# Optimization experiments

Hardware: AMD Instinct MI355X
Metric: run time of the kernel (lower is better)

The kernel has to match this reference:

```python
import jax, jax.numpy as jnp
import numpy as np

N_NODES = 50000
N_EDGES = 800000
HIDDEN = 128
BN_EPS = 1e-5
LEAKY_SLOPE = 0.01


def setup_inputs() -> dict:
    key = jax.random.key(0)
    ks = jax.random.split(key, 8)
    x = jax.random.normal(ks[0], (N_NODES, HIDDEN), dtype=jnp.float32)
    edge_index = jax.random.randint(ks[1], (2, N_EDGES), 0, N_NODES, dtype=jnp.int64)
    # stacked per-layer params (4 SAGEConv layers, all 128->128)
    sc = 1.0 / np.sqrt(HIDDEN)
    Wl = jax.random.normal(ks[2], (4, HIDDEN, HIDDEN), dtype=jnp.float32) * sc
    bl = jax.random.normal(ks[3], (4, HIDDEN), dtype=jnp.float32) * sc
    Wr = jax.random.normal(ks[4], (4, HIDDEN, HIDDEN), dtype=jnp.float32) * sc
    gamma = jnp.ones((4, HIDDEN), dtype=jnp.float32)
    beta = jnp.zeros((4, HIDDEN), dtype=jnp.float32)
    return {"x": x, "edge_index": edge_index, "Wl": Wl, "bl": bl,
            "Wr": Wr, "gamma": gamma, "beta": beta}


def _sage_mean_agg(x, src, dst, n):
    # gather source features per edge, scatter-mean onto destination nodes
    msg = x[src]                                                  # [E, F]
    agg = jax.ops.segment_sum(msg, dst, num_segments=n)           # [N, F]
    cnt = jax.ops.segment_sum(jnp.ones_like(dst, dtype=x.dtype), dst, num_segments=n)
    return agg / jnp.maximum(cnt, 1.0)[:, None]


def _bn_train(x, g, b):
    mu = jnp.mean(x, axis=0)
    var = jnp.mean((x - mu) ** 2, axis=0)  # biased variance (PyTorch BN normalization)
    return (x - mu) * jax.lax.rsqrt(var + BN_EPS) * g + b


def reference(x, edge_index, Wl, bl, Wr, gamma, beta):
    src, dst = edge_index[0], edge_index[1]
    n = x.shape[0]
    h = x
    for i in range(4):
        agg = _sage_mean_agg(h, src, dst, n)
        h = agg @ Wl[i] + bl[i] + h @ Wr[i]          # SAGEConv: lin_l(mean_nbr) + lin_r(root)
        h = jnp.where(h >= 0, h, LEAKY_SLOPE * h)    # leaky_relu
        h = _bn_train(h, gamma[i], beta[i])
    # dropout: eval-mode identity (deterministic reference)
    return h
```

## Files before the change

### kernel.cpp

```cpp
#include <hip/hip_runtime.h>
#include <hip/hip_bf16.h>

#define N_NODES 50000
#define N_EDGES 800000
#define F 128
#define BN_EPS 1e-5f
#define SLOPE 0.01f
#define NB 782
#define CAP 64
#define NBIN 128
#define BINSZ 391
#define QCAP2 8192
#define ABLK 512
#define AITER 7
#define PB1 6250
#define PB2 512

typedef __attribute__((ext_vector_type(8))) __bf16 bf16x8_t;
typedef __attribute__((ext_vector_type(8))) unsigned short u16x8_t;
typedef __attribute__((ext_vector_type(4))) float f32x4_t;

__device__ __forceinline__ unsigned short f2b(float f) {
    unsigned int u = __float_as_uint(f);
    unsigned int r = (u + 0x7fffu + ((u >> 16) & 1u)) >> 16;
    return (unsigned short)r;
}
__device__ __forceinline__ float b2f_lo(unsigned int v) { return __uint_as_float(v << 16); }
__device__ __forceinline__ float b2f_hi(unsigned int v) { return __uint_as_float(v & 0xffff0000u); }


__global__ __launch_bounds__(256) void bucket2_kernel(const int* __restrict__ src,
                                                      const int* __restrict__ dst,
                                                      int* __restrict__ qtail,
                                                      unsigned int* __restrict__ qdata) {
    __shared__ int counts[NBIN];
    __shared__ int cur[NBIN];
    __shared__ int base[NBIN];
    const int tid = threadIdx.x;

    for (int k = tid; k < NBIN; k += 256) { counts[k] = 0; cur[k] = 0; }
    __syncthreads();

    unsigned int pack[AITER];
    int bin[AITER];
    const int stride = ABLK * 256;
#pragma unroll
    for (int it = 0; it < AITER; ++it) {
        const int e = blockIdx.x * 256 + tid + it * stride;
        bin[it] = -1;
        if (e < N_EDGES) {
            int d = __builtin_nontemporal_load(dst + e);
            int s = __builtin_nontemporal_load(src + e);
            bin[it] = d / BINSZ;
            pack[it] = ((unsigned int)d << 16) | (unsigned int)s;
            atomicAdd(&counts[bin[it]], 1);
        }
    }
    __syncthreads();
    if (tid < NBIN) {
        int c = counts[tid];
        base[tid] = (c > 0) ? atomicAdd(&qtail[tid * 16], c) : 0;
    }
    __syncthreads();
#pragma unroll
    for (int it = 0; it < AITER; ++it) {
        if (bin[it] >= 0) {
            int slot = base[bin[it]] + atomicAdd(&cur[bin[it]], 1);
            qdata[(long)bin[it] * QCAP2 + slot] = pack[it];
        }
    }
}

__global__ __launch_bounds__(256) void scatter2_kernel(const unsigned int* __restrict__ qdata,
                                                       const int* __restrict__ qtail,
                                                       int* __restrict__ deg,
                                                       unsigned short* __restrict__ csr) {
    __shared__ int cnt[BINSZ];
    __shared__ unsigned short stage[BINSZ][CAP];
    const int b = blockIdx.x;
    const int nbase = b * BINSZ;
    const int nn = min(BINSZ, N_NODES - nbase);
    const int tid = threadIdx.x;

    for (int r = tid; r < BINSZ; r += 256) cnt[r] = 0;
    __syncthreads();

    const int n = qtail[b * 16];
    const unsigned int* q = qdata + (long)b * QCAP2;
    for (int i = tid; i < n; i += 256) {
        unsigned int p = q[i];
        int local = (int)(p >> 16) - nbase;
        int pos = atomicAdd(&cnt[local], 1);
        if (pos < CAP) stage[local][pos] = (unsigned short)(p & 0xffff);
    }
    __syncthreads();

    for (int c = tid; c < nn * (CAP / 8); c += 256) {
        const int r = c >> 3;
        const int col = (c & 7) * 8;
        *(u16x8_t*)(csr + (long)(nbase + r) * CAP + col) = *(const u16x8_t*)&stage[r][col];
    }
    for (int r = tid; r < nn; r += 256) deg[nbase + r] = min(cnt[r], CAP);
}


__global__ __launch_bounds__(256) void prep_kernel(const float* __restrict__ x,
                                                   unsigned short* __restrict__ hb,
                                                   const float* __restrict__ Wl,
                                                   const float* __restrict__ Wr,
                                                   unsigned short* __restrict__ Wt,
                                                   float* __restrict__ scale,
                                                   float* __restrict__ shift) {
    const int b = blockIdx.x;
    const int tid = threadIdx.x;
    if (b < PB1) {
        long i = (long)b * 256 + tid;
        float4 v = ((const float4*)x)[i];
        ushort4 o;
        o.x = f2b(v.x); o.y = f2b(v.y); o.z = f2b(v.z); o.w = f2b(v.w);
        ((ushort4*)hb)[i] = o;
    } else if (b < PB1 + PB2) {
        int idx = (b - PB1) * 256 + tid;
        int k = idx & 255;
        int n = (idx >> 8) & 127;
        int i = idx >> 15;
        float v = (k < F) ? Wl[((long)i * F + k) * F + n]
                          : Wr[((long)i * F + (k - F)) * F + n];
        Wt[idx] = f2b(v);
    } else {
        if (tid < F) { scale[tid] = 1.f; shift[tid] = 0.f; }
    }
}


__device__ __forceinline__ u16x8_t affine8(u16x8_t av, const float* __restrict__ sc,
                                           const float* __restrict__ sh) {
    u16x8_t r;
#pragma unroll
    for (int j = 0; j < 8; ++j) {
        float v = __uint_as_float(((unsigned int)av[j]) << 16);
        v = v * sc[j] + sh[j];
        r[j] = f2b(v);
    }
    return r;
}

#define ACC8(A, V)                               \
    A[0] += b2f_lo(V.x); A[1] += b2f_hi(V.x);    \
    A[2] += b2f_lo(V.y); A[3] += b2f_hi(V.y);    \
    A[4] += b2f_lo(V.z); A[5] += b2f_hi(V.z);    \
    A[6] += b2f_lo(V.w); A[7] += b2f_hi(V.w);

#define PACKJ(j, A) {                                                   \
    const float4 s0 = *(const float4*)(scale + q * 8 + 32 * (j));       \
    const float4 s1 = *(const float4*)(scale + q * 8 + 32 * (j) + 4);   \
    const float4 t0 = *(const float4*)(shift + q * 8 + 32 * (j));       \
    const float4 t1 = *(const float4*)(shift + q * 8 + 32 * (j) + 4);   \
    u16x8_t r;                                                          \
    r[0] = f2b(A[0] * inv * s0.x + t0.x);                               \
    r[1] = f2b(A[1] * inv * s0.y + t0.y);                               \
    r[2] = f2b(A[2] * inv * s0.z + t0.z);                               \
    r[3] = f2b(A[3] * inv * s0.w + t0.w);                               \
    r[4] = f2b(A[4] * inv * s1.x + t1.x);                               \
    r[5] = f2b(A[5] * inv * s1.y + t1.y);                               \
    r[6] = f2b(A[6] * inv * s1.z + t1.z);                               \
    r[7] = f2b(A[7] * inv * s1.w + t1.w);                               \
    areg[j] = r; }

#if __has_builtin(__builtin_amdgcn_global_load_lds)
#define STAGE_HALF(half) {                                                        \
    _Pragma("unroll")                                                             \
    for (int f = 0; f < 8; ++f) {                                                 \
        const int fid = f * 256 + tid;                                            \
        const int lf = fid & 63;                                                  \
        const int ksf = (fid >> 6) & 3;                                           \
        const int ntf = fid >> 8;                                                 \
        const int n = ntf * 16 + (lf & 15);                                       \
        const int k = (half) * 128 + ksf * 32 + (lf >> 4) * 8;                    \
        const unsigned short* gsrc = Wt + (long)n * 256 + k;                      \
        unsigned short* lbase = stage + (f * 256 + wave * 64) * 8;                \
        __builtin_amdgcn_global_load_lds(                                         \
            (const __attribute__((address_space(1))) void*)gsrc,                  \
            (__attribute__((address_space(3))) void*)lbase, 16, 0, 0);            \
    } }
#else
#define STAGE_HALF(half) {                                                        \
    _Pragma("unroll")                                                             \
    for (int f = 0; f < 8; ++f) {                                                 \
        const int fid = f * 256 + tid;                                            \
        const int lf = fid & 63;                                                  \
        const int ksf = (fid >> 6) & 3;                                           \
        const int ntf = fid >> 8;                                                 \
        const int n = ntf * 16 + (lf & 15);                                       \
        const int k = (half) * 128 + ksf * 32 + (lf >> 4) * 8;                    \
        const unsigned short* gsrc = Wt + (long)n * 256 + k;                      \
        *(u16x8_t*)(stage + fid * 8) = *(const u16x8_t*)gsrc;                     \
    } }
#endif

__global__ __launch_bounds__(256) void gemm_fused(const unsigned short* __restrict__ hin,
                                                  const int* __restrict__ deg,
                                                  const unsigned short* __restrict__ csr,
                                                  const float* __restrict__ scale,
                                                  const float* __restrict__ shift,
                                                  const unsigned short* __restrict__ Wt,
                                                  const float* __restrict__ bl,
                                                  unsigned short* __restrict__ Pb,
                                                  float* __restrict__ partial) {
    __shared__ __align__(16) char shraw[32768];
    unsigned short* stage = (unsigned short*)shraw;
    unsigned short* ep16 = (unsigned short*)shraw;
    __shared__ float lsum[4][F];
    __shared__ float lsq[4][F];

    const int tid = threadIdx.x;
    const int wave = tid >> 6, lane = tid & 63;
    const int m = lane & 15, q = lane >> 4;
    const int rbase = blockIdx.x * 64 + wave * 16;
    const int arow = rbase + m;
    const bool aval = arow < N_NODES;

    STAGE_HALF(0);

    const unsigned short* hp = hin + (long)arow * F + q * 8;
    u16x8_t hraw[4];
#pragma unroll
    for (int j = 0; j < 4; ++j) hraw[j] = (u16x8_t)0;
    if (aval) {
#pragma unroll
        for (int j = 0; j < 4; ++j) hraw[j] = *(const u16x8_t*)(hp + j * 32);
    }

    const int d = aval ? deg[arow] : 0;
    const unsigned short* crow = csr + (long)arow * CAP;
    const unsigned short* hq = hin + q * 8;
    float a0[8], a1[8], a2[8], a3[8];
#pragma unroll
    for (int j = 0; j < 8; ++j) { a0[j] = 0.f; a1[j] = 0.f; a2[j] = 0.f; a3[j] = 0.f; }

    const int d4 = d & ~3;
    for (int e = 0; e < d4; e += 4) {
        const ushort4 iv = *(const ushort4*)(crow + e);
        const unsigned short* r0 = hq + (long)iv.x * F;
        const unsigned short* r1 = hq + (long)iv.y * F;
        const unsigned short* r2 = hq + (long)iv.z * F;
        const unsigned short* r3 = hq + (long)iv.w * F;
        uint4 v00 = *(const uint4*)(r0);
        uint4 v01 = *(const uint4*)(r0 + 32);
        uint4 v02 = *(const uint4*)(r0 + 64);
        uint4 v03 = *(const uint4*)(r0 + 96);
        uint4 v10 = *(const uint4*)(r1);
        uint4 v11 = *(const uint4*)(r1 + 32);
        uint4 v12 = *(const uint4*)(r1 + 64);
        uint4 v13 = *(const uint4*)(r1 + 96);
        uint4 v20 = *(const uint4*)(r2);
        uint4 v21 = *(const uint4*)(r2 + 32);
        uint4 v22 = *(const uint4*)(r2 + 64);
        uint4 v23 = *(const uint4*)(r2 + 96);
        uint4 v30 = *(const uint4*)(r3);
        uint4 v31 = *(const uint4*)(r3 + 32);
        uint4 v32 = *(const uint4*)(r3 + 64);
        uint4 v33 = *(const uint4*)(r3 + 96);
        ACC8(a0, v00); ACC8(a1, v01); ACC8(a2, v02); ACC8(a3, v03);
        ACC8(a0, v10); ACC8(a1, v11); ACC8(a2, v12); ACC8(a3, v13);
        ACC8(a0, v20); ACC8(a1, v21); ACC8(a2, v22); ACC8(a3, v23);
        ACC8(a0, v30); ACC8(a1, v31); ACC8(a2, v32); ACC8(a3, v33);
    }
    for (int e = d4; e < d; ++e) {
        const int s = (int)crow[e];
        const unsigned short* hr = hq + (long)s * F;
        uint4 v0 = *(const uint4*)(hr);
        uint4 v1 = *(const uint4*)(hr + 32);
        uint4 v2 = *(const uint4*)(hr + 64);
        uint4 v3 = *(const uint4*)(hr + 96);
        ACC8(a0, v0);
        ACC8(a1, v1);
        ACC8(a2, v2);
        ACC8(a3, v3);
    }

    u16x8_t areg[8];
#pragma unroll
    for (int j = 0; j < 8; ++j) areg[j] = (u16x8_t)0;
    if (d > 0) {
        const float inv = 1.0f / (float)d;
        PACKJ(0, a0);
        PACKJ(1, a1);
        PACKJ(2, a2);
        PACKJ(3, a3);
    }
    if (aval) {
#pragma unroll
        for (int j = 0; j < 4; ++j) {
            const int base = j * 32 + q * 8;
            areg[4 + j] = affine8(hraw[j], scale + base, shift + base);
        }
    }

    f32x4_t acc[8];
#pragma unroll
    for (int nt = 0; nt < 8; ++nt) acc[nt] = (f32x4_t){0.f, 0.f, 0.f, 0.f};

    __syncthreads();
#pragma unroll
    for (int ks = 0; ks < 4; ++ks) {
        bf16x8_t af = __builtin_bit_cast(bf16x8_t, areg[ks]);
#pragma unroll
        for (int nt = 0; nt < 8; ++nt) {
            u16x8_t bv = *(const u16x8_t*)(stage + ((nt * 4 + ks) * 64 + lane) * 8);
            bf16x8_t bf = __builtin_bit_cast(bf16x8_t, bv);
            acc[nt] = __builtin_amdgcn_mfma_f32_16x16x32_bf16(af, bf, acc[nt], 0, 0, 0);
        }
    }
    __syncthreads();
    STAGE_HALF(1);
    __syncthreads();
#pragma unroll
    for (int ks = 0; ks < 4; ++ks) {
        bf16x8_t af = __builtin_bit_cast(bf16x8_t, areg[4 + ks]);
#pragma unroll
        for (int nt = 0; nt < 8; ++nt) {
            u16x8_t bv = *(const u16x8_t*)(stage + ((nt * 4 + ks) * 64 + lane) * 8);
            bf16x8_t bf = __builtin_bit_cast(bf16x8_t, bv);
            acc[nt] = __builtin_amdgcn_mfma_f32_16x16x32_bf16(af, bf, acc[nt], 0, 0, 0);
        }
    }

    __syncthreads();

    float cs[8], cq[8];
#pragma unroll
    for (int nt = 0; nt < 8; ++nt) {
        cs[nt] = 0.f; cq[nt] = 0.f;
        const int c = nt * 16 + m;
        const float b = bl[c];
#pragma unroll
        for (int r = 0; r < 4; ++r) {
            const int rl = wave * 16 + q * 4 + r;
            float v = acc[nt][r] + b;
            v = (v >= 0.f) ? v : SLOPE * v;
            ep16[rl * 136 + c] = f2b(v);
            if (rbase + q * 4 + r < N_NODES) {
                cs[nt] += v;
                cq[nt] += v * v;
            }
        }
    }

    {
        const int rq = lane >> 4;
        const int cc = (lane & 15) * 8;
#pragma unroll
        for (int r2 = 0; r2 < 4; ++r2) {
            const int rl = wave * 16 + rq * 4 + r2;
            const int grow = blockIdx.x * 64 + rl;
            if (grow < N_NODES)
                *(u16x8_t*)(Pb + (long)grow * F + cc) = *(const u16x8_t*)(ep16 + rl * 136 + cc);
        }
    }

#pragma unroll
    for (int nt = 0; nt < 8; ++nt) {
        cs[nt] += __shfl_xor(cs[nt], 16);
        cs[nt] += __shfl_xor(cs[nt], 32);
        cq[nt] += __shfl_xor(cq[nt], 16);
        cq[nt] += __shfl_xor(cq[nt], 32);
    }
    if (lane < 16) {
#pragma unroll
        for (int nt = 0; nt < 8; ++nt) {
            lsum[wave][nt * 16 + m] = cs[nt];
            lsq[wave][nt * 16 + m] = cq[nt];
        }
    }
    __syncthreads();
    if (tid < F) {
        float s = 0.f, s2 = 0.f;
#pragma unroll
        for (int w = 0; w < 4; ++w) {
            s += lsum[w][tid];
            s2 += lsq[w][tid];
        }
        partial[(long)blockIdx.x * 256 + tid] = s;
        partial[(long)blockIdx.x * 256 + 128 + tid] = s2;
    }
}

__global__ __launch_bounds__(256) void bn_reduce(const float* __restrict__ partial,
                                                 const float* __restrict__ gamma,
                                                 const float* __restrict__ beta,
                                                 float* __restrict__ scale,
                                                 float* __restrict__ shift) {
    const int j = blockIdx.x;
    const int t = threadIdx.x;
    const int lane = t & 63, wave = t >> 6;
    float s = 0.f, s2 = 0.f;
    for (int b = t; b < NB; b += 256) {
        s += partial[(long)b * 256 + j];
        s2 += partial[(long)b * 256 + 128 + j];
    }
#pragma unroll
    for (int off = 1; off < 64; off <<= 1) {
        s += __shfl_xor(s, off);
        s2 += __shfl_xor(s2, off);
    }
    __shared__ float ls[4], lq[4];
    if (lane == 0) { ls[wave] = s; lq[wave] = s2; }
    __syncthreads();
    if (t == 0) {
        float S = ls[0] + ls[1] + ls[2] + ls[3];
        float Q = lq[0] + lq[1] + lq[2] + lq[3];
        const float inv_n = 1.0f / (float)N_NODES;
        float mu = S * inv_n;
        float var = Q * inv_n - mu * mu;
        float scl = gamma[j] * rsqrtf(var + BN_EPS);
        scale[j] = scl;
        shift[j] = beta[j] - mu * scl;
    }
}

__global__ __launch_bounds__(256) void bn_apply_f(const unsigned short* __restrict__ Pb,
                                                  float* __restrict__ out,
                                                  const float* __restrict__ scale,
                                                  const float* __restrict__ shift) {
    long i = (long)blockIdx.x * blockDim.x + threadIdx.x;
    if (i >= (long)N_NODES * (F / 8)) return;
    const int c8 = (int)(i & 15);
    uint4 v = ((const uint4*)Pb)[i];
    const float4 sc0 = ((const float4*)scale)[c8 * 2];
    const float4 sc1 = ((const float4*)scale)[c8 * 2 + 1];
    const float4 sh0 = ((const float4*)shift)[c8 * 2];
    const float4 sh1 = ((const float4*)shift)[c8 * 2 + 1];
    float4 o0, o1;
    o0.x = b2f_lo(v.x) * sc0.x + sh0.x;
    o0.y = b2f_hi(v.x) * sc0.y + sh0.y;
    o0.z = b2f_lo(v.y) * sc0.z + sh0.z;
    o0.w = b2f_hi(v.y) * sc0.w + sh0.w;
    o1.x = b2f_lo(v.z) * sc1.x + sh1.x;
    o1.y = b2f_hi(v.z) * sc1.y + sh1.y;
    o1.z = b2f_lo(v.w) * sc1.z + sh1.z;
    o1.w = b2f_hi(v.w) * sc1.w + sh1.w;
    ((float4*)out)[i * 2] = o0;
    ((float4*)out)[i * 2 + 1] = o1;
}


extern "C" void kernel_launch(void* const* d_in, const int* in_sizes, int n_in,
                              void* d_out, int out_size, void* d_ws, size_t ws_size,
                              hipStream_t stream) {
    const float* x     = (const float*)d_in[0];
    const int*   ei    = (const int*)d_in[1];
    const float* Wl    = (const float*)d_in[2];
    const float* bl    = (const float*)d_in[3];
    const float* Wr    = (const float*)d_in[4];
    const float* gamma = (const float*)d_in[5];
    const float* beta  = (const float*)d_in[6];
    float* out = (float*)d_out;

    const int* src = ei;
    const int* dst = ei + N_EDGES;

    char* w = (char*)d_ws;
    auto alloc = [&](size_t bytes) -> char* {
        char* p = w;
        w += (bytes + 255) & ~(size_t)255;
        return p;
    };
    unsigned short* hbA   = (unsigned short*)alloc((size_t)N_NODES * F * 2);
    unsigned short* hbB   = (unsigned short*)alloc((size_t)N_NODES * F * 2);
    unsigned short* Wt    = (unsigned short*)alloc((size_t)4 * F * 256 * 2);
    int*   deg      = (int*)alloc((size_t)N_NODES * 4);
    int*   qtail    = (int*)alloc((size_t)NBIN * 16 * 4);
    unsigned int* qdata = (unsigned int*)alloc((size_t)NBIN * QCAP2 * 4);
    unsigned short* csr = (unsigned short*)alloc((size_t)N_NODES * CAP * 2);
    float* partial  = (float*)alloc((size_t)NB * 256 * 4);
    float* scale    = (float*)alloc(F * 4);
    float* shift    = (float*)alloc(F * 4);

    hipMemsetAsync(qtail, 0, (size_t)NBIN * 16 * 4, stream);

    bucket2_kernel<<<ABLK, 256, 0, stream>>>(src, dst, qtail, qdata);
    scatter2_kernel<<<NBIN, 256, 0, stream>>>(qdata, qtail, deg, csr);
    prep_kernel<<<PB1 + PB2 + 1, 256, 0, stream>>>(x, hbA, Wl, Wr, Wt, scale, shift);

    const int n8 = N_NODES * (F / 8);

    unsigned short* hin = hbA;
    unsigned short* hnext = hbB;
    for (int i = 0; i < 4; ++i) {
        gemm_fused<<<NB, 256, 0, stream>>>(
            hin, deg, csr, scale, shift, Wt + (size_t)i * F * 256, bl + (size_t)i * F,
            hnext, partial);

        bn_reduce<<<F, 256, 0, stream>>>(partial, gamma + (size_t)i * F, beta + (size_t)i * F,
                                         scale, shift);

        unsigned short* t = hin; hin = hnext; hnext = t;
    }
    bn_apply_f<<<(n8 + 255) / 256, 256, 0, stream>>>(hin, out, scale, shift);
}
```

Measured before the change: 374.5 us.

## Split neighbor aggregation of each 16-row tile across four waves

Each block now handles 16 rows instead of 64, so the grid grows from 782 to 3125 blocks. The four waves split every row's neighbor list into quarters and combine their partial sums with LDS float atomics. Each wave then computes two of the eight output column tiles in the MFMA GEMM. The aim is more parallelism on the latency-bound gather and better load balance across uneven node degrees. In exchange, the 64 KB of weights are staged into LDS four times as often per row, LDS atomics are added, and bn_reduce has more partial rows to sum.

After: 994.9 us. 166% more time.

```diff
diff --git a/kernel.cpp b/kernel.cpp
--- a/kernel.cpp
+++ b/kernel.cpp
@@ -6,7 +6,7 @@
 #define F 128
 #define BN_EPS 1e-5f
 #define SLOPE 0.01f
-#define NB 782
+#define NB2 3125
 #define CAP 64
 #define NBIN 128
 #define BINSZ 391
@@ -76,7 +76,7 @@
                                                        int* __restrict__ deg,
                                                        unsigned short* __restrict__ csr) {
     __shared__ int cnt[BINSZ];
-    __shared__ unsigned short stage[BINSZ][CAP];
+    __shared__ __align__(16) unsigned short stage[BINSZ][CAP];
     const int b = blockIdx.x;
     const int nbase = b * BINSZ;
     const int nn = min(BINSZ, N_NODES - nbase);
@@ -150,22 +150,6 @@
     A[2] += b2f_lo(V.y); A[3] += b2f_hi(V.y);    \
     A[4] += b2f_lo(V.z); A[5] += b2f_hi(V.z);    \
     A[6] += b2f_lo(V.w); A[7] += b2f_hi(V.w);
-
-#define PACKJ(j, A) {                                                   \
-    const float4 s0 = *(const float4*)(scale + q * 8 + 32 * (j));       \
-    const float4 s1 = *(const float4*)(scale + q * 8 + 32 * (j) + 4);   \
-    const float4 t0 = *(const float4*)(shift + q * 8 + 32 * (j));       \
-    const float4 t1 = *(const float4*)(shift + q * 8 + 32 * (j) + 4);   \
-    u16x8_t r;                                                          \
-    r[0] = f2b(A[0] * inv * s0.x + t0.x);                               \
-    r[1] = f2b(A[1] * inv * s0.y + t0.y);                               \
-    r[2] = f2b(A[2] * inv * s0.z + t0.z);                               \
-    r[3] = f2b(A[3] * inv * s0.w + t0.w);                               \
-    r[4] = f2b(A[4] * inv * s1.x + t1.x);                               \
-    r[5] = f2b(A[5] * inv * s1.y + t1.y);                               \
-    r[6] = f2b(A[6] * inv * s1.z + t1.z);                               \
-    r[7] = f2b(A[7] * inv * s1.w + t1.w);                               \
-    areg[j] = r; }
 
 #if __has_builtin(__builtin_amdgcn_global_load_lds)
 #define STAGE_HALF(half) {                                                        \
@@ -198,48 +182,45 @@
     } }
 #endif
 
-__global__ __launch_bounds__(256) void gemm_fused(const unsigned short* __restrict__ hin,
-                                                  const int* __restrict__ deg,
-                                                  const unsigned short* __restrict__ csr,
-                                                  const float* __restrict__ scale,
-                                                  const float* __restrict__ shift,
-                                                  const unsigned short* __restrict__ Wt,
-                                                  const float* __restrict__ bl,
-                                                  unsigned short* __restrict__ Pb,
-                                                  float* __restrict__ partial) {
+__global__ __launch_bounds__(256, 4) void gemm_fused(const unsigned short* __restrict__ hin,
+                                                     const int* __restrict__ deg,
+                                                     const unsigned short* __restrict__ csr,
+                                                     const float* __restrict__ scale,
+                                                     const float* __restrict__ shift,
+                                                     const unsigned short* __restrict__ Wt,
+                                                     const float* __restrict__ bl,
+                                                     unsigned short* __restrict__ Pb,
+                                                     float* __restrict__ partial) {
     __shared__ __align__(16) char shraw[32768];
+    __shared__ __align__(16) float ldsA[2048];
     unsigned short* stage = (unsigned short*)shraw;
-    unsigned short* ep16 = (unsigned short*)shraw;
-    __shared__ float lsum[4][F];
-    __shared__ float lsq[4][F];
+    unsigned short* ep16 = (unsigned short*)ldsA;
 
     const int tid = threadIdx.x;
     const int wave = tid >> 6, lane = tid & 63;
     const int m = lane & 15, q = lane >> 4;
-    const int rbase = blockIdx.x * 64 + wave * 16;
+    const int rbase = blockIdx.x * 16;
     const int arow = rbase + m;
-    const bool aval = arow < N_NODES;
+
+    for (int i = tid; i < 2048; i += 256) ldsA[i] = 0.f;
+    __syncthreads();
 
     STAGE_HALF(0);
 
-    const unsigned short* hp = hin + (long)arow * F + q * 8;
-    u16x8_t hraw[4];
-#pragma unroll
-    for (int j = 0; j < 4; ++j) hraw[j] = (u16x8_t)0;
-    if (aval) {
-#pragma unroll
-        for (int j = 0; j < 4; ++j) hraw[j] = *(const u16x8_t*)(hp + j * 32);
-    }
-
-    const int d = aval ? deg[arow] : 0;
+    const int d = deg[arow];
     const unsigned short* crow = csr + (long)arow * CAP;
     const unsigned short* hq = hin + q * 8;
+
     float a0[8], a1[8], a2[8], a3[8];
 #pragma unroll
     for (int j = 0; j < 8; ++j) { a0[j] = 0.f; a1[j] = 0.f; a2[j] = 0.f; a3[j] = 0.f; }
 
-    const int d4 = d & ~3;
-    for (int e = 0; e < d4; e += 4) {
+    const int qlen = ((d + 15) >> 4) << 2;
+    const int lo = min(wave * qlen, d);
+    const int hi = min(lo + qlen, d);
+    const int nfull = lo + ((hi - lo) & ~3);
+    int e = lo;
+    for (; e < nfull; e += 4) {
         const ushort4 iv = *(const ushort4*)(crow + e);
         const unsigned short* r0 = hq + (long)iv.x * F;
         const unsigned short* r1 = hq + (long)iv.y * F;
@@ -266,123 +247,119 @@
         ACC8(a0, v20); ACC8(a1, v21); ACC8(a2, v22); ACC8(a3, v23);
         ACC8(a0, v30); ACC8(a1, v31); ACC8(a2, v32); ACC8(a3, v33);
     }
-    for (int e = d4; e < d; ++e) {
+    for (; e < hi; ++e) {
         const int s = (int)crow[e];
         const unsigned short* hr = hq + (long)s * F;
         uint4 v0 = *(const uint4*)(hr);
         uint4 v1 = *(const uint4*)(hr + 32);
         uint4 v2 = *(const uint4*)(hr + 64);
         uint4 v3 = *(const uint4*)(hr + 96);
-        ACC8(a0, v0);
-        ACC8(a1, v1);
-        ACC8(a2, v2);
-        ACC8(a3, v3);
-    }
+        ACC8(a0, v0); ACC8(a1, v1); ACC8(a2, v2); ACC8(a3, v3);
+    }
+
+#pragma unroll
+    for (int c = 0; c < 8; ++c) {
+        atomicAdd(&ldsA[(q * 8 + c) * 16 + m], a0[c]);
+        atomicAdd(&ldsA[(q * 8 + 32 + c) * 16 + m], a1[c]);
+        atomicAdd(&ldsA[(q * 8 + 64 + c) * 16 + m], a2[c]);
+        atomicAdd(&ldsA[(q * 8 + 96 + c) * 16 + m], a3[c]);
+    }
+
+    __syncthreads();
 
     u16x8_t areg[8];
 #pragma unroll
     for (int j = 0; j < 8; ++j) areg[j] = (u16x8_t)0;
     if (d > 0) {
         const float inv = 1.0f / (float)d;
-        PACKJ(0, a0);
-        PACKJ(1, a1);
-        PACKJ(2, a2);
-        PACKJ(3, a3);
-    }
-    if (aval) {
 #pragma unroll
         for (int j = 0; j < 4; ++j) {
-            const int base = j * 32 + q * 8;
-            areg[4 + j] = affine8(hraw[j], scale + base, shift + base);
+            const int fb = q * 8 + 32 * j;
+            const float4 s0 = *(const float4*)(scale + fb);
+            const float4 s1 = *(const float4*)(scale + fb + 4);
+            const float4 t0 = *(const float4*)(shift + fb);
+            const float4 t1 = *(const float4*)(shift + fb + 4);
+            u16x8_t r;
+            r[0] = f2b(ldsA[(fb + 0) * 16 + m] * inv * s0.x + t0.x);
+            r[1] = f2b(ldsA[(fb + 1) * 16 + m] * inv * s0.y + t0.y);
+            r[2] = f2b(ldsA[(fb + 2) * 16 + m] * inv * s0.z + t0.z);
+            r[3] = f2b(ldsA[(fb + 3) * 16 + m] * inv * s0.w + t0.w);
+            r[4] = f2b(ldsA[(fb + 4) * 16 + m] * inv * s1.x + t1.x);
+            r[5] = f2b(ldsA[(fb + 5) * 16 + m] * inv * s1.y + t1.y);
+            r[6] = f2b(ldsA[(fb + 6) * 16 + m] * inv * s1.z + t1.z);
+            r[7] = f2b(ldsA[(fb + 7) * 16 + m] * inv * s1.w + t1.w);
+            areg[j] = r;
         }
     }
 
-    f32x4_t acc[8];
-#pragma unroll
-    for (int nt = 0; nt < 8; ++nt) acc[nt] = (f32x4_t){0.f, 0.f, 0.f, 0.f};
-
-    __syncthreads();
+    const int nt0 = wave * 2, nt1 = wave * 2 + 1;
+    f32x4_t acc0 = (f32x4_t){0.f, 0.f, 0.f, 0.f};
+    f32x4_t acc1 = (f32x4_t){0.f, 0.f, 0.f, 0.f};
+
 #pragma unroll
     for (int ks = 0; ks < 4; ++ks) {
         bf16x8_t af = __builtin_bit_cast(bf16x8_t, areg[ks]);
-#pragma unroll
-        for (int nt = 0; nt < 8; ++nt) {
-            u16x8_t bv = *(const u16x8_t*)(stage + ((nt * 4 + ks) * 64 + lane) * 8);
-            bf16x8_t bf = __builtin_bit_cast(bf16x8_t, bv);
-            acc[nt] = __builtin_amdgcn_mfma_f32_16x16x32_bf16(af, bf, acc[nt], 0, 0, 0);
-        }
-    }
-    __syncthreads();
+        u16x8_t b0 = *(const u16x8_t*)(stage + ((nt0 * 4 + ks) * 64 + lane) * 8);
+        u16x8_t b1 = *(const u16x8_t*)(stage + ((nt1 * 4 + ks) * 64 + lane) * 8);
+        acc0 = __builtin_amdgcn_mfma_f32_16x16x32_bf16(af, __builtin_bit_cast(bf16x8_t, b0), acc0, 0, 0, 0);
+        acc1 = __builtin_amdgcn_mfma_f32_16x16x32_bf16(af, __builtin_bit_cast(bf16x8_t, b1), acc1, 0, 0, 0);
+    }
+    __syncthreads();
+
+    const unsigned short* hp = hin + (long)arow * F + q * 8;
+    u16x8_t hraw[4];
+#pragma unroll
+    for (int j = 0; j < 4; ++j) hraw[j] = *(const u16x8_t*)(hp + j * 32);
     STAGE_HALF(1);
-    __syncthreads();
+#pragma unroll
+    for (int j = 0; j < 4; ++j) {
+        const int fb = j * 32 + q * 8;
+        areg[4 + j] = affine8(hraw[j], scale + fb, shift + fb);
+    }
+    __syncthreads();
+
 #pragma unroll
     for (int ks = 0; ks < 4; ++ks) {
         bf16x8_t af = __builtin_bit_cast(bf16x8_t, areg[4 + ks]);
-#pragma unroll
-        for (int nt = 0; nt < 8; ++nt) {
-            u16x8_t bv = *(const u16x8_t*)(stage + ((nt * 4 + ks) * 64 + lane) * 8);
-            bf16x8_t bf = __builtin_bit_cast(bf16x8_t, bv);
-            acc[nt] = __builtin_amdgcn_mfma_f32_16x16x32_bf16(af, bf, acc[nt], 0, 0, 0);
-        }
-    }
-
-    __syncthreads();
-
-    float cs[8], cq[8];
-#pragma unroll
-    for (int nt = 0; nt < 8; ++nt) {
-        cs[nt] = 0.f; cq[nt] = 0.f;
-        const int c = nt * 16 + m;
-        const float b = bl[c];
-#pragma unroll
-        for (int r = 0; r < 4; ++r) {
-            const int rl = wave * 16 + q * 4 + r;
-            float v = acc[nt][r] + b;
-            v = (v >= 0.f) ? v : SLOPE * v;
-            ep16[rl * 136 + c] = f2b(v);
-            if (rbase + q * 4 + r < N_NODES) {
-                cs[nt] += v;
-                cq[nt] += v * v;
-            }
-        }
-    }
+        u16x8_t b0 = *(const u16x8_t*)(stage + ((nt0 * 4 + ks) * 64 + lane) * 8);
+        u16x8_t b1 = *(const u16x8_t*)(stage + ((nt1 * 4 + ks) * 64 + lane) * 8);
+        acc0 = __builtin_amdgcn_mfma_f32_16x16x32_bf16(af, __builtin_bit_cast(bf16x8_t, b0), acc0, 0, 0, 0);
+        acc1 = __builtin_amdgcn_mfma_f32_16x16x32_bf16(af, __builtin_bit_cast(bf16x8_t, b1), acc1, 0, 0, 0);
+    }
+    __syncthreads();
+
+    float cs0 = 0.f, cq0 = 0.f, cs1 = 0.f, cq1 = 0.f;
+    const float b0 = bl[nt0 * 16 + m];
+    const float b1 = bl[nt1 * 16 + m];
+#pragma unroll
+    for (int r = 0; r < 4; ++r) {
+        const int rl = q * 4 + r;
+        float v0 = acc0[r] + b0;
+        v0 = (v0 >= 0.f) ? v0 : SLOPE * v0;
+        float v1 = acc1[r] + b1;
+        v1 = (v1 >= 0.f) ? v1 : SLOPE * v1;
+        ep16[rl * 136 + nt0 * 16 + m] = f2b(v0);
+        ep16[rl * 136 + nt1 * 16 + m] = f2b(v1);
+        cs0 += v0; cq0 += v0 * v0;
+        cs1 += v1; cq1 += v1 * v1;
+    }
+    cs0 += __shfl_xor(cs0, 16); cs0 += __shfl_xor(cs0, 32);
+    cq0 += __shfl_xor(cq0, 16); cq0 += __shfl_xor(cq0, 32);
+    cs1 += __shfl_xor(cs1, 16); cs1 += __shfl_xor(cs1, 32);
+    cq1 += __shfl_xor(cq1, 16); cq1 += __shfl_xor(cq1, 32);
+    if (lane < 16) {
+        float* pb = partial + (long)blockIdx.x * 256;
+        pb[nt0 * 16 + lane] = cs0;
+        pb[nt1 * 16 + lane] = cs1;
+        pb[128 + nt0 * 16 + lane] = cq0;
+        pb[128 + nt1 * 16 + lane] = cq1;
+    }
+    __syncthreads();
 
     {
-        const int rq = lane >> 4;
-        const int cc = (lane & 15) * 8;
-#pragma unroll
-        for (int r2 = 0; r2 < 4; ++r2) {
-            const int rl = wave * 16 + rq * 4 + r2;
-            const int grow = blockIdx.x * 64 + rl;
-            if (grow < N_NODES)
-                *(u16x8_t*)(Pb + (long)grow * F + cc) = *(const u16x8_t*)(ep16 + rl * 136 + cc);
-        }
-    }
-
-#pragma unroll
-    for (int nt = 0; nt < 8; ++nt) {
-        cs[nt] += __shfl_xor(cs[nt], 16);
-        cs[nt] += __shfl_xor(cs[nt], 32);
-        cq[nt] += __shfl_xor(cq[nt], 16);
-        cq[nt] += __shfl_xor(cq[nt], 32);
-    }
-    if (lane < 16) {
-#pragma unroll
-        for (int nt = 0; nt < 8; ++nt) {
-            lsum[wave][nt * 16 + m] = cs[nt];
-            lsq[wave][nt * 16 + m] = cq[nt];
-        }
-    }
-    __syncthreads();
-    if (tid < F) {
-        float s = 0.f, s2 = 0.f;
-#pragma unroll
-        for (int w = 0; w < 4; ++w) {
-            s += lsum[w][tid];
-            s2 += lsq[w][tid];
-        }
-        partial[(long)blockIdx.x * 256 + tid] = s;
-        partial[(long)blockIdx.x * 256 + 128 + tid] = s2;
+        const int row = tid >> 4, ch = tid & 15;
+        *(u16x8_t*)(Pb + (long)(rbase + row) * F + ch * 8) =
+            *(const u16x8_t*)(ep16 + row * 136 + ch * 8);
     }
 }
 
@@ -395,7 +372,7 @@
     const int t = threadIdx.x;
     const int lane = t & 63, wave = t >> 6;
     float s = 0.f, s2 = 0.f;
-    for (int b = t; b < NB; b += 256) {
+    for (int b = t; b < NB2; b += 256) {
         s += partial[(long)b * 256 + j];
         s2 += partial[(long)b * 256 + 128 + j];
     }
@@ -473,7 +450,7 @@
     int*   qtail    = (int*)alloc((size_t)NBIN * 16 * 4);
     unsigned int* qdata = (unsigned int*)alloc((size_t)NBIN * QCAP2 * 4);
     unsigned short* csr = (unsigned short*)alloc((size_t)N_NODES * CAP * 2);
-    float* partial  = (float*)alloc((size_t)NB * 256 * 4);
+    float* partial  = (float*)alloc((size_t)NB2 * 256 * 4);
     float* scale    = (float*)alloc(F * 4);
     float* shift    = (float*)alloc(F * 4);
 
@@ -488,7 +465,7 @@
     unsigned short* hin = hbA;
     unsigned short* hnext = hbB;
     for (int i = 0; i < 4; ++i) {
-        gemm_fused<<<NB, 256, 0, stream>>>(
+        gemm_fused<<<NB2, 256, 0, stream>>>(
             hin, deg, csr, scale, shift, Wt + (size_t)i * F * 256, bl + (size_t)i * F,
             hnext, partial);
 
```
